# Kernel tuning notes

Measured on AMD Instinct MI355X. Metric: run time of the kernel, lower is better.

Reference implementation:

```python
import jax, jax.numpy as jnp
import numpy as np

N_NODES = 50000
N_EDGES = 800000
D_IN = 128
D_OUT = 128
K = 3


def setup_inputs() -> dict:
    key = jax.random.key(0)
    k1, k2, k3, k4 = jax.random.split(key, 4)
    x = jax.random.normal(k1, (N_NODES, D_IN), dtype=jnp.float32)
    W = jax.random.normal(k2, (K, D_IN, D_OUT), dtype=jnp.float32) * 0.05
    edge_index = jax.random.randint(k3, (K, 2, N_EDGES), 0, N_NODES, dtype=jnp.int32)
    edge_weight = jax.random.uniform(k4, (K, N_EDGES), dtype=jnp.float32)
    return {"x": x, "W": W, "edge_index": edge_index, "edge_weight": edge_weight}


def reference(x, W, edge_index, edge_weight):
    # ChebConv: out = sum_k A_k @ (x @ W_k), A_k given as weighted edge lists.
    n = x.shape[0]
    out = jnp.zeros((n, W.shape[-1]), dtype=x.dtype)
    for k in range(W.shape[0]):
        h = x @ W[k]                                   # [N, D_OUT] dense GEMM
        src = edge_index[k, 0]
        dst = edge_index[k, 1]
        msg = h[src] * edge_weight[k][:, None]         # [E, D_OUT] gather + scale
        out = out + jax.ops.segment_sum(msg, dst, num_segments=n)
    return out
```

## Files before the change

### kernel.cpp

```cpp
#include <hip/hip_runtime.h>
#include <hip/hip_bf16.h>

#define N_NODES 50000
#define N_EDGES 800000
#define D 128
#define KCHEB 3
#define M_CNT (KCHEB * N_NODES)
#define NBKT 98
#define TOTB (KCHEB * NBKT)
#define SLAB 16384
#define EPB 2048
#define NBLK_E ((N_EDGES + EPB - 1) / EPB)

typedef __attribute__((ext_vector_type(8))) short short8v;
typedef __attribute__((ext_vector_type(4))) float f32x4;

__device__ inline unsigned f2bf(float f) {
    unsigned x = __float_as_uint(f);
    unsigned r = ((x >> 16) & 1u) + 0x7FFFu;
    return (x + r) >> 16;
}

__global__ __launch_bounds__(256) void gemm_mfma(const float* __restrict__ x,
                                                 const float* __restrict__ Wall,
                                                 unsigned* __restrict__ h3, int n) {
    __shared__ unsigned short Wt[128 * 128];
    const int t = threadIdx.x;
    const float* W = Wall + (size_t)blockIdx.y * D * D;
    unsigned* h2 = h3 + (size_t)blockIdx.y * N_NODES * 64;

    #pragma unroll 4
    for (int i = 0; i < 16; ++i) {
        int linear = i * 256 + t;
        int r  = linear >> 5;
        int c4 = (linear & 31) * 4;
        float4 wv = *(const float4*)&W[r * 128 + c4];
        #pragma unroll
        for (int j = 0; j < 4; ++j) {
            int row = c4 + j;
            int byte_in_row = (r * 2) ^ ((row & 7) << 4);
            Wt[row * 128 + (byte_in_row >> 1)] = (unsigned short)f2bf((&wv.x)[j]);
        }
    }
    __syncthreads();

    const int lane = t & 63, w = t >> 6;
    const int m0 = blockIdx.x * 64 + w * 16;
    const int arow = m0 + (lane & 15);
    const float* xr = x + (size_t)(arow < n ? arow : 0) * D + ((lane >> 4) << 3);

    short8v afr[4];
    #pragma unroll
    for (int kt = 0; kt < 4; ++kt) {
        float4 p0 = *(const float4*)(xr + kt * 32);
        float4 p1 = *(const float4*)(xr + kt * 32 + 4);
        union { short8v s; unsigned u[4]; } a;
        a.u[0] = f2bf(p0.x) | (f2bf(p0.y) << 16);
        a.u[1] = f2bf(p0.z) | (f2bf(p0.w) << 16);
        a.u[2] = f2bf(p1.x) | (f2bf(p1.y) << 16);
        a.u[3] = f2bf(p1.z) | (f2bf(p1.w) << 16);
        afr[kt] = a.s;
    }

    f32x4 acc[8] = {};
    const int kb = (lane >> 4) << 4;
    #pragma unroll
    for (int nn = 0; nn < 8; ++nn) {
        const int row = nn * 16 + (lane & 15);
        const int sw = (row & 7) << 4;
        const unsigned short* wr = &Wt[row * 128];
        #pragma unroll
        for (int kt = 0; kt < 4; ++kt) {
            int byte_in_row = ((kt << 6) + kb) ^ sw;
            short8v b = *(const short8v*)&wr[byte_in_row >> 1];
            acc[nn] = __builtin_amdgcn_mfma_f32_16x16x32_bf16(afr[kt], b, acc[nn], 0, 0, 0);
        }
    }

    unsigned short* hs = (unsigned short*)h2;
    const int orow_base = m0 + ((lane >> 4) << 2);
    const int col_base = lane & 15;
    #pragma unroll
    for (int nn = 0; nn < 8; ++nn) {
        int col = nn * 16 + col_base;
        #pragma unroll
        for (int r = 0; r < 4; ++r) {
            int orow = orow_base + r;
            if (orow < n) hs[(size_t)orow * D + col] = (unsigned short)f2bf(acc[nn][r]);
        }
    }
}

__global__ __launch_bounds__(256) void bucket_bin(const int* __restrict__ ei,
                                                  const float* __restrict__ ew,
                                                  int* __restrict__ cursor,
                                                  uint2* __restrict__ binned) {
    __shared__ int lh[NBKT], gb[NBKT], lc[NBKT];
    const int k = blockIdx.y, t = threadIdx.x;
    for (int i = t; i < NBKT; i += 256) { lh[i] = 0; lc[i] = 0; }
    __syncthreads();
    const int* srcs = ei + (size_t)k * 2 * N_EDGES;
    const int* dsts = srcs + N_EDGES;
    const float* w = ew + (size_t)k * N_EDGES;
    const int base = blockIdx.x * EPB;
    #pragma unroll
    for (int q = 0; q < EPB / 1024; ++q) {
        int e = base + q * 1024 + t * 4;
        if (e < N_EDGES) {
            int4 d4 = *(const int4*)&dsts[e];
            atomicAdd(&lh[d4.x >> 9], 1);
            atomicAdd(&lh[d4.y >> 9], 1);
            atomicAdd(&lh[d4.z >> 9], 1);
            atomicAdd(&lh[d4.w >> 9], 1);
        }
    }
    __syncthreads();
    for (int i = t; i < NBKT; i += 256)
        gb[i] = lh[i] ? atomicAdd(&cursor[k * NBKT + i], lh[i]) : 0;
    __syncthreads();
    #pragma unroll
    for (int q = 0; q < EPB / 1024; ++q) {
        int e = base + q * 1024 + t * 4;
        if (e < N_EDGES) {
            int4 d4 = *(const int4*)&dsts[e];
            int4 s4 = *(const int4*)&srcs[e];
            float4 w4 = *(const float4*)&w[e];
            #pragma unroll
            for (int j = 0; j < 4; ++j) {
                int d = (&d4.x)[j];
                int b = d >> 9;
                int pos = (k * NBKT + b) * SLAB + gb[b] + atomicAdd(&lc[b], 1);
                binned[pos] = make_uint2(__float_as_uint((&w4.x)[j]),
                                         (unsigned)(&s4.x)[j] | ((unsigned)(d & 511) << 16));
            }
        }
    }
}

__global__ __launch_bounds__(256) void build_csr(const uint2* __restrict__ binned,
                                                 const int* __restrict__ cursor,
                                                 int* __restrict__ off,
                                                 int* __restrict__ num,
                                                 int2* __restrict__ csr) {
    __shared__ int nh[512], ex[512], wsum[4];
    const int kb = blockIdx.x;
    const int k = kb / NBKT, b = kb % NBKT;
    const int t = threadIdx.x;
    const int beg = kb * SLAB;
    const int end = beg + cursor[kb];

    for (int i = t; i < 512; i += 256) nh[i] = 0;
    __syncthreads();
    for (int i = beg + t; i < end; i += 256)
        atomicAdd(&nh[(binned[i].y >> 16) & 511], 1);
    __syncthreads();

    int a0 = nh[2 * t], a1 = nh[2 * t + 1];
    int s = a0 + a1;
    int lane = t & 63, wid = t >> 6;
    int v = s;
    #pragma unroll
    for (int d = 1; d < 64; d <<= 1) {
        int u = __shfl_up(v, d, 64);
        if (lane >= d) v += u;
    }
    if (lane == 63) wsum[wid] = v;
    __syncthreads();
    int wb = 0;
    for (int i = 0; i < wid; ++i) wb += wsum[i];
    int ep = wb + v - s;
    ex[2 * t] = ep;
    ex[2 * t + 1] = ep + a0;

    const int node0 = b * 512;
    int n0 = node0 + 2 * t, n1 = node0 + 2 * t + 1;
    if (n0 < N_NODES) { off[k * N_NODES + n0] = beg + ep;      num[k * N_NODES + n0] = a0; }
    if (n1 < N_NODES) { off[k * N_NODES + n1] = beg + ep + a0; num[k * N_NODES + n1] = a1; }

    for (int i = t; i < 512; i += 256) nh[i] = 0;
    __syncthreads();
    for (int i = beg + t; i < end; i += 256) {
        uint2 e = binned[i];
        int dl = (e.y >> 16) & 511;
        int pos = beg + ex[dl] + atomicAdd(&nh[dl], 1);
        csr[pos] = make_int2((int)(e.y & 0xFFFFu), (int)e.x);
    }
}

__global__ __launch_bounds__(256) void gather_all(const unsigned* __restrict__ h3,
                                                  const int2* __restrict__ csr,
                                                  const int* __restrict__ off,
                                                  const int* __restrict__ num,
                                                  float* __restrict__ out) {
    const int wid = threadIdx.x >> 6;
    const int lane = threadIdx.x & 63;
    const int node = blockIdx.x * 4 + wid;
    if (node >= N_NODES) return;

    float ax = 0.f, ay = 0.f;
    #pragma unroll
    for (int k = 0; k < KCHEB; ++k) {
        const unsigned* h2 = h3 + (size_t)k * N_NODES * 64;
        const int kd = k * N_NODES + node;
        int i = off[kd];
        const int end = i + num[kd];
        for (; i + 8 <= end; i += 8) {
            int2 ed[8];
            unsigned u[8];
            #pragma unroll
            for (int j = 0; j < 8; ++j) ed[j] = csr[i + j];
            #pragma unroll
            for (int j = 0; j < 8; ++j) u[j] = h2[(size_t)ed[j].x * 64 + lane];
            #pragma unroll
            for (int j = 0; j < 8; ++j) {
                float w = __int_as_float(ed[j].y);
                ax += w * __uint_as_float(u[j] << 16);
                ay += w * __uint_as_float(u[j] & 0xFFFF0000u);
            }
        }
        for (; i < end; ++i) {
            int2 e = csr[i];
            float w = __int_as_float(e.y);
            unsigned uu = h2[(size_t)e.x * 64 + lane];
            ax += w * __uint_as_float(uu << 16);
            ay += w * __uint_as_float(uu & 0xFFFF0000u);
        }
    }
    *(float2*)&out[(size_t)node * D + lane * 2] = make_float2(ax, ay);
}

extern "C" void kernel_launch(void* const* d_in, const int* in_sizes, int n_in,
                              void* d_out, int out_size, void* d_ws, size_t ws_size,
                              hipStream_t stream) {
    const float* x  = (const float*)d_in[0];
    const float* W  = (const float*)d_in[1];
    const int*   ei = (const int*)d_in[2];
    const float* ew = (const float*)d_in[3];
    float* out = (float*)d_out;

    char* ws = (char*)d_ws;
    int2*     csr    = (int2*)    (ws);
    uint2*    binned = (uint2*)   (ws + 38535168);
    unsigned* h3     = (unsigned*)(ws + 77070336);
    int*      off    = (int*)     (ws + 115470336);
    int*      num    = (int*)     (ws + 116070336);
    int*      cursor = (int*)     (ws + 116670336);

    hipMemsetAsync(cursor, 0, TOTB * sizeof(int), stream);

    const dim3 egrid(NBLK_E, KCHEB);
    bucket_bin<<<egrid, 256, 0, stream>>>(ei, ew, cursor, binned);

    const dim3 ggrid((N_NODES + 63) / 64, KCHEB);
    gemm_mfma<<<ggrid, 256, 0, stream>>>(x, W, h3, N_NODES);

    build_csr<<<TOTB, 256, 0, stream>>>(binned, cursor, off, num, csr);

    const int gat_grid = (N_NODES + 3) / 4;
    gather_all<<<gat_grid, 256, 0, stream>>>(h3, csr, off, num, out);
}
```

Baseline: 296.9 us.

## Pack CSR entries into 32 bits, widen gather lanes, precompute bf16 weights

```diff
diff --git a/kernel.cpp b/kernel.cpp
--- a/kernel.cpp
+++ b/kernel.cpp
@@ -5,7 +5,6 @@
 #define N_EDGES 800000
 #define D 128
 #define KCHEB 3
-#define M_CNT (KCHEB * N_NODES)
 #define NBKT 98
 #define TOTB (KCHEB * NBKT)
 #define SLAB 16384
@@ -21,26 +20,36 @@
     return (x + r) >> 16;
 }
 
+__global__ __launch_bounds__(256) void wprep(const float* __restrict__ W,
+                                             unsigned short* __restrict__ Wtg) {
+    const int k = blockIdx.x;
+    const float* Wk = W + (size_t)k * D * D;
+    unsigned short* o = Wtg + (size_t)k * D * D;
+    for (int i = threadIdx.x; i < 4096; i += 256) {
+        int r  = i >> 5;
+        int c4 = (i & 31) * 4;
+        float4 wv = *(const float4*)&Wk[r * 128 + c4];
+        #pragma unroll
+        for (int j = 0; j < 4; ++j) {
+            int row = c4 + j;
+            int byte_in_row = (r * 2) ^ ((row & 7) << 4);
+            o[row * 128 + (byte_in_row >> 1)] = (unsigned short)f2bf((&wv.x)[j]);
+        }
+    }
+}
+
 __global__ __launch_bounds__(256) void gemm_mfma(const float* __restrict__ x,
-                                                 const float* __restrict__ Wall,
+                                                 const unsigned short* __restrict__ Wtg,
                                                  unsigned* __restrict__ h3, int n) {
     __shared__ unsigned short Wt[128 * 128];
     const int t = threadIdx.x;
-    const float* W = Wall + (size_t)blockIdx.y * D * D;
     unsigned* h2 = h3 + (size_t)blockIdx.y * N_NODES * 64;
 
-    #pragma unroll 4
-    for (int i = 0; i < 16; ++i) {
-        int linear = i * 256 + t;
-        int r  = linear >> 5;
-        int c4 = (linear & 31) * 4;
-        float4 wv = *(const float4*)&W[r * 128 + c4];
-        #pragma unroll
-        for (int j = 0; j < 4; ++j) {
-            int row = c4 + j;
-            int byte_in_row = (r * 2) ^ ((row & 7) << 4);
-            Wt[row * 128 + (byte_in_row >> 1)] = (unsigned short)f2bf((&wv.x)[j]);
-        }
+    {
+        const uint4* src = (const uint4*)(Wtg + (size_t)blockIdx.y * D * D);
+        uint4* dst = (uint4*)Wt;
+        #pragma unroll
+        for (int i = 0; i < 8; ++i) dst[t + 256 * i] = src[t + 256 * i];
     }
     __syncthreads();
 
@@ -141,7 +150,7 @@
                                                  const int* __restrict__ cursor,
                                                  int* __restrict__ off,
                                                  int* __restrict__ num,
-                                                 int2* __restrict__ csr) {
+                                                 unsigned* __restrict__ csr4) {
     __shared__ int nh[512], ex[512], wsum[4];
     const int kb = blockIdx.x;
     const int k = kb / NBKT, b = kb % NBKT;
@@ -183,21 +192,21 @@
         uint2 e = binned[i];
         int dl = (e.y >> 16) & 511;
         int pos = beg + ex[dl] + atomicAdd(&nh[dl], 1);
-        csr[pos] = make_int2((int)(e.y & 0xFFFFu), (int)e.x);
+        csr4[pos] = (e.y & 0xFFFFu) | (f2bf(__uint_as_float(e.x)) << 16);
     }
 }
 
 __global__ __launch_bounds__(256) void gather_all(const unsigned* __restrict__ h3,
-                                                  const int2* __restrict__ csr,
+                                                  const unsigned* __restrict__ csr4,
                                                   const int* __restrict__ off,
                                                   const int* __restrict__ num,
                                                   float* __restrict__ out) {
-    const int wid = threadIdx.x >> 6;
-    const int lane = threadIdx.x & 63;
-    const int node = blockIdx.x * 4 + wid;
+    const int half = threadIdx.x >> 5;
+    const int l = threadIdx.x & 31;
+    const int node = blockIdx.x * 8 + half;
     if (node >= N_NODES) return;
 
-    float ax = 0.f, ay = 0.f;
+    float a0 = 0.f, a1 = 0.f, a2 = 0.f, a3 = 0.f;
     #pragma unroll
     for (int k = 0; k < KCHEB; ++k) {
         const unsigned* h2 = h3 + (size_t)k * N_NODES * 64;
@@ -205,28 +214,33 @@
         int i = off[kd];
         const int end = i + num[kd];
         for (; i + 8 <= end; i += 8) {
-            int2 ed[8];
-            unsigned u[8];
-            #pragma unroll
-            for (int j = 0; j < 8; ++j) ed[j] = csr[i + j];
-            #pragma unroll
-            for (int j = 0; j < 8; ++j) u[j] = h2[(size_t)ed[j].x * 64 + lane];
+            unsigned e[8];
+            uint2 u[8];
+            #pragma unroll
+            for (int j = 0; j < 8; ++j) e[j] = csr4[i + j];
+            #pragma unroll
+            for (int j = 0; j < 8; ++j)
+                u[j] = *(const uint2*)&h2[(size_t)(e[j] & 0xFFFFu) * 64 + l * 2];
             #pragma unroll
             for (int j = 0; j < 8; ++j) {
-                float w = __int_as_float(ed[j].y);
-                ax += w * __uint_as_float(u[j] << 16);
-                ay += w * __uint_as_float(u[j] & 0xFFFF0000u);
+                float w = __uint_as_float(e[j] & 0xFFFF0000u);
+                a0 += w * __uint_as_float(u[j].x << 16);
+                a1 += w * __uint_as_float(u[j].x & 0xFFFF0000u);
+                a2 += w * __uint_as_float(u[j].y << 16);
+                a3 += w * __uint_as_float(u[j].y & 0xFFFF0000u);
             }
         }
         for (; i < end; ++i) {
-            int2 e = csr[i];
-            float w = __int_as_float(e.y);
-            unsigned uu = h2[(size_t)e.x * 64 + lane];
-            ax += w * __uint_as_float(uu << 16);
-            ay += w * __uint_as_float(uu & 0xFFFF0000u);
-        }
-    }
-    *(float2*)&out[(size_t)node * D + lane * 2] = make_float2(ax, ay);
+            unsigned e = csr4[i];
+            float w = __uint_as_float(e & 0xFFFF0000u);
+            uint2 u = *(const uint2*)&h2[(size_t)(e & 0xFFFFu) * 64 + l * 2];
+            a0 += w * __uint_as_float(u.x << 16);
+            a1 += w * __uint_as_float(u.x & 0xFFFF0000u);
+            a2 += w * __uint_as_float(u.y << 16);
+            a3 += w * __uint_as_float(u.y & 0xFFFF0000u);
+        }
+    }
+    *(float4*)&out[(size_t)node * D + l * 4] = make_float4(a0, a1, a2, a3);
 }
 
 extern "C" void kernel_launch(void* const* d_in, const int* in_sizes, int n_in,
@@ -239,23 +253,26 @@
     float* out = (float*)d_out;
 
     char* ws = (char*)d_ws;
-    int2*     csr    = (int2*)    (ws);
-    uint2*    binned = (uint2*)   (ws + 38535168);
-    unsigned* h3     = (unsigned*)(ws + 77070336);
-    int*      off    = (int*)     (ws + 115470336);
-    int*      num    = (int*)     (ws + 116070336);
-    int*      cursor = (int*)     (ws + 116670336);
+    unsigned*       csr4   = (unsigned*)      (ws);
+    uint2*          binned = (uint2*)         (ws + 19267584);
+    unsigned*       h3     = (unsigned*)      (ws + 57802752);
+    int*            off    = (int*)           (ws + 96202752);
+    int*            num    = (int*)           (ws + 96802752);
+    int*            cursor = (int*)           (ws + 97402752);
+    unsigned short* Wtg    = (unsigned short*)(ws + 97403936);
 
     hipMemsetAsync(cursor, 0, TOTB * sizeof(int), stream);
+
+    wprep<<<KCHEB, 256, 0, stream>>>(W, Wtg);
 
     const dim3 egrid(NBLK_E, KCHEB);
     bucket_bin<<<egrid, 256, 0, stream>>>(ei, ew, cursor, binned);
 
     const dim3 ggrid((N_NODES + 63) / 64, KCHEB);
-    gemm_mfma<<<ggrid, 256, 0, stream>>>(x, W, h3, N_NODES);
-
-    build_csr<<<TOTB, 256, 0, stream>>>(binned, cursor, off, num, csr);
-
-    const int gat_grid = (N_NODES + 3) / 4;
-    gather_all<<<gat_grid, 256, 0, stream>>>(h3, csr, off, num, out);
-}
+    gemm_mfma<<<ggrid, 256, 0, stream>>>(x, Wtg, h3, N_NODES);
+
+    build_csr<<<TOTB, 256, 0, stream>>>(binned, cursor, off, num, csr4);
+
+    const int gat_grid = (N_NODES + 7) / 8;
+    gather_all<<<gat_grid, 256, 0, stream>>>(h3, csr4, off, num, out);
+}
```

Measured after the change: 264.5 us. 10.9% less time.
